# Optimization experiments

Measured on AMD Instinct MI355X. Metric: run time of the kernel, lower is better.

The kernel has to match this reference:

```python
import jax, jax.numpy as jnp
import numpy as np

N_NODES = 100000
N_EDGES = 1600000
N_GRAPHS = 64
D_IN, D_HID, D_LAT = 2, 64, 32


def setup_inputs() -> dict:
    key = jax.random.key(0)
    k1, k2, k3, k4, k5, k6, k7 = jax.random.split(key, 7)
    x = jax.random.normal(k1, (N_NODES, D_IN), dtype=jnp.float32)
    edge_index = jax.random.randint(k2, (2, N_EDGES), 0, N_NODES, dtype=jnp.int64)
    batch = jnp.sort(jax.random.randint(k3, (N_NODES,), 0, N_GRAPHS, dtype=jnp.int64))
    # GCNConv params (glorot-ish scale)
    W1 = jax.random.normal(k4, (D_IN, D_HID), dtype=jnp.float32) * (1.0 / np.sqrt(D_IN))
    b1 = jnp.zeros((D_HID,), dtype=jnp.float32)
    W2 = jax.random.normal(k5, (D_HID, D_LAT), dtype=jnp.float32) * (1.0 / np.sqrt(D_HID))
    b2 = jnp.zeros((D_LAT,), dtype=jnp.float32)
    return {"x": x, "W1": W1, "b1": b1, "W2": W2, "b2": b2,
            "edge_index": edge_index, "batch": batch}


def _gcn_conv(x, W, b, src, dst, n_nodes):
    """PyG GCNConv: add self-loops, symmetric deg^-1/2 normalization, linear, scatter-add."""
    h = x @ W  # [N, d_out]
    loop = jnp.arange(n_nodes, dtype=src.dtype)
    src_f = jnp.concatenate([src, loop])
    dst_f = jnp.concatenate([dst, loop])
    deg = jax.ops.segment_sum(jnp.ones_like(dst_f, dtype=h.dtype), dst_f,
                              num_segments=n_nodes)  # in-degree incl. self-loop
    dis = jnp.where(deg > 0, jax.lax.rsqrt(deg), 0.0)
    norm = dis[src_f] * dis[dst_f]  # [E+N]
    msg = h[src_f] * norm[:, None]  # edge gather (memory-bound)
    out = jax.ops.segment_sum(msg, dst_f, num_segments=n_nodes)
    return out + b


def reference(x, W1, b1, W2, b2, edge_index, batch):
    src, dst = edge_index[0], edge_index[1]
    n = x.shape[0]
    h = jax.nn.relu(_gcn_conv(x, W1, b1, src, dst, n))
    z = _gcn_conv(h, W2, b2, src, dst, n)
    # global_mean_pool over graph ids
    sums = jax.ops.segment_sum(z, batch, num_segments=N_GRAPHS)
    cnts = jax.ops.segment_sum(jnp.ones((n,), dtype=z.dtype), batch,
                               num_segments=N_GRAPHS)
    return sums / jnp.maximum(cnts, 1.0)[:, None]
```

## Files before the change

### kernel.cpp

```cpp
#include <hip/hip_runtime.h>
#include <hip/hip_fp16.h>

#define N_NODES  100000
#define N_EDGES  1600000
#define N_GRAPHS 64
#define NBUCK    391
#define NBLK     256
#define CHUNK    (N_EDGES / NBLK)
#define NODEBLK  1563

#define OFF_GSTART 0
#define OFF_ROWPTR 128
#define OFF_DIS    100224
#define OFF_S      200320
#define OFF_CSR    400384
#define OFF_QLO    2000384
#define OFF_QHI    2800512
#define OFF_BHIST  2000384
#define OFF_BOFFL  2100736
#define OFF_BSUM   2201088
#define OFF_BSTART 2201600
#define OFF_TMP    2202112

__device__ __forceinline__ int excl_scan_256(int v, int* wsum) {
  int t = threadIdx.x, lane = t & 63, w = t >> 6;
  int x = v;
#pragma unroll
  for (int off = 1; off < 64; off <<= 1) {
    int y = __shfl_up(x, off, 64);
    if (lane >= off) x += y;
  }
  if (lane == 63) wsum[w] = x;
  __syncthreads();
  if (t == 0) {
    int r = 0;
#pragma unroll
    for (int i = 0; i < 4; ++i) { int tv = wsum[i]; wsum[i] = r; r += tv; }
  }
  __syncthreads();
  return x - v + wsum[w];
}

__device__ __forceinline__ int excl_scan_512(int v, int* wsum) {
  int t = threadIdx.x, lane = t & 63, w = t >> 6;
  int x = v;
#pragma unroll
  for (int off = 1; off < 64; off <<= 1) {
    int y = __shfl_up(x, off, 64);
    if (lane >= off) x += y;
  }
  if (lane == 63) wsum[w] = x;
  __syncthreads();
  if (t == 0) {
    int r = 0;
#pragma unroll
    for (int i = 0; i < 8; ++i) { int tv = wsum[i]; wsum[i] = r; r += tv; }
  }
  __syncthreads();
  return x - v + wsum[w];
}

__global__ void k_hist(const int* __restrict__ dst, int* __restrict__ bhist) {
  __shared__ int hist[NBUCK];
  int t = threadIdx.x, k = blockIdx.x;
  for (int b = t; b < NBUCK; b += 256) hist[b] = 0;
  __syncthreads();
  int e0 = k * CHUNK, e1 = e0 + CHUNK;
  for (int e = e0 + t; e < e1; e += 256) atomicAdd(&hist[dst[e] >> 8], 1);
  __syncthreads();
  for (int b = t; b < NBUCK; b += 256) bhist[b * NBLK + k] = hist[b];
}

__global__ void k_scan_a(const int* __restrict__ bhist, int* __restrict__ boffl,
                         int* __restrict__ bsum, const int* __restrict__ batch,
                         int* __restrict__ gstart) {
  __shared__ int wsum[4];
  int t = threadIdx.x, b = blockIdx.x;
  int i = b * 256 + t;
  if (i < N_NODES) {
    int bi = batch[i];
    if (i == 0) {
      for (int g = 0; g <= bi; ++g) gstart[g] = 0;
    } else {
      int bp = batch[i - 1];
      for (int g = bp + 1; g <= bi; ++g) gstart[g] = i;
    }
    if (i == N_NODES - 1) {
      for (int g = bi + 1; g <= N_GRAPHS; ++g) gstart[g] = N_NODES;
    }
  }
  int v = bhist[b * NBLK + t];
  int ex = excl_scan_256(v, wsum);
  boffl[b * NBLK + t] = ex;
  if (t == NBLK - 1) bsum[b] = ex + v;
}

__global__ void k_scan_b(const int* __restrict__ bsum, int* __restrict__ bstart,
                         float* __restrict__ pooled) {
  __shared__ int wsum[8];
  int t = threadIdx.x;
  for (int i = t; i < N_GRAPHS * 32; i += 512) pooled[i] = 0.f;
  int v = (t < NBUCK) ? bsum[t] : 0;
  int ex = excl_scan_512(v, wsum);
  if (t <= NBUCK) bstart[t] = ex;
}

__global__ void k_scatter(const int* __restrict__ src, const int* __restrict__ dst,
                          const int* __restrict__ bstart, const int* __restrict__ boffl,
                          int* __restrict__ tmp) {
  __shared__ int sbase[NBUCK];
  __shared__ int fill[NBUCK];
  int t = threadIdx.x, k = blockIdx.x;
  for (int b = t; b < NBUCK; b += 256) {
    sbase[b] = bstart[b] + boffl[b * NBLK + k];
    fill[b] = 0;
  }
  __syncthreads();
  int e0 = k * CHUNK, e1 = e0 + CHUNK;
  for (int e = e0 + t; e < e1; e += 256) {
    int s_ = src[e], d_ = dst[e];
    int b = d_ >> 8;
    int pos = sbase[b] + atomicAdd(&fill[b], 1);
    tmp[pos] = (s_ << 8) | (d_ & 255);
  }
}

__global__ void k_fine(const int* __restrict__ tmp, const int* __restrict__ bstart,
                       const float* __restrict__ x, int* __restrict__ csr_src,
                       int* __restrict__ row_ptr, float* __restrict__ dis,
                       float2* __restrict__ s) {
  __shared__ int hist[256];
  __shared__ int fill[256];
  __shared__ int wsum[4];
  int t = threadIdx.x, b = blockIdx.x;
  int base_n = b << 8;
  int e0 = bstart[b], e1 = bstart[b + 1];
  hist[t] = 0;
  __syncthreads();
  for (int e = e0 + t; e < e1; e += 256) atomicAdd(&hist[tmp[e] & 255], 1);
  __syncthreads();
  int h = hist[t];
  int ex = excl_scan_256(h, wsum);
  hist[t] = ex;
  fill[t] = 0;
  int nn = min(256, N_NODES - base_n);
  if (t < nn) {
    int v = base_n + t;
    row_ptr[v] = e0 + ex;
    float dv = rsqrtf((float)(h + 1));
    dis[v] = dv;
    float2 xv = ((const float2*)x)[v];
    s[v] = make_float2(xv.x * dv, xv.y * dv);
  }
  if (b == NBUCK - 1 && t == 0) row_ptr[N_NODES] = e1;
  __syncthreads();
  for (int e = e0 + t; e < e1; e += 256) {
    int p = tmp[e];
    int fine = p & 255;
    int pos = e0 + hist[fine] + atomicAdd(&fill[fine], 1);
    csr_src[pos] = p >> 8;
  }
}

__global__ void k_layer1(const float2* __restrict__ s, const float* __restrict__ dis,
                         const int* __restrict__ row_ptr, const int* __restrict__ csr_src,
                         const float* __restrict__ W1, const float* __restrict__ b1,
                         const float* __restrict__ W2, int4* __restrict__ q_lo,
                         int4* __restrict__ q_hi) {
  __shared__ float4 sWB[64];
  __shared__ float4 sW2[512];
  int tid = threadIdx.x;
  if (tid < 64) sWB[tid] = make_float4(W1[tid], W1[64 + tid], b1[tid], 0.f);
  for (int i = tid; i < 512; i += 256) sW2[i] = ((const float4*)W2)[i];
  __syncthreads();
  int v = blockIdx.x * 256 + tid;
  if (v >= N_NODES) return;
  int beg = row_ptr[v], end = row_ptr[v + 1];
  float2 sv = s[v];
  float t0 = sv.x, t1 = sv.y;
  int k = beg;
  for (; k + 4 <= end; k += 4) {
    int u0 = csr_src[k], u1 = csr_src[k + 1], u2 = csr_src[k + 2], u3 = csr_src[k + 3];
    float2 a = s[u0], b = s[u1], c = s[u2], d = s[u3];
    t0 += (a.x + b.x) + (c.x + d.x);
    t1 += (a.y + b.y) + (c.y + d.y);
  }
  for (; k < end; ++k) {
    float2 su = s[csr_src[k]];
    t0 += su.x;
    t1 += su.y;
  }
  float dv = dis[v];
  t0 *= dv;
  t1 *= dv;
  float4 a4[8];
#pragma unroll
  for (int m = 0; m < 8; ++m) a4[m] = make_float4(0.f, 0.f, 0.f, 0.f);
  for (int j = 0; j < 64; ++j) {
    float4 wb = sWB[j];
    float r = fmaxf(fmaf(t0, wb.x, fmaf(t1, wb.y, wb.z)), 0.f);
#pragma unroll
    for (int m = 0; m < 8; ++m) {
      float4 w = sW2[j * 8 + m];
      a4[m].x = fmaf(r, w.x, a4[m].x);
      a4[m].y = fmaf(r, w.y, a4[m].y);
      a4[m].z = fmaf(r, w.z, a4[m].z);
      a4[m].w = fmaf(r, w.w, a4[m].w);
    }
  }
  int pk[16];
#pragma unroll
  for (int m = 0; m < 8; ++m) {
    __half2 h0 = __floats2half2_rn(a4[m].x * dv, a4[m].y * dv);
    __half2 h1 = __floats2half2_rn(a4[m].z * dv, a4[m].w * dv);
    pk[2 * m]     = *reinterpret_cast<int*>(&h0);
    pk[2 * m + 1] = *reinterpret_cast<int*>(&h1);
  }
  q_lo[v * 2]     = make_int4(pk[0], pk[1], pk[2], pk[3]);
  q_lo[v * 2 + 1] = make_int4(pk[4], pk[5], pk[6], pk[7]);
  q_hi[v * 2]     = make_int4(pk[8], pk[9], pk[10], pk[11]);
  q_hi[v * 2 + 1] = make_int4(pk[12], pk[13], pk[14], pk[15]);
}

__global__ void k_layer2(const __half2* __restrict__ q_lo, const __half2* __restrict__ q_hi,
                         const float* __restrict__ dis, const int* __restrict__ row_ptr,
                         const int* __restrict__ csr_src, const int* __restrict__ batch,
                         float* __restrict__ pooled) {
  __shared__ float2 red[32][8];
  int w = blockIdx.x;
  int h = (w & 7) >> 2;
  int sub = (w >> 3) * 4 + (w & 3);
  if (sub >= NODEBLK) return;
  const __half2* q = h ? q_hi : q_lo;
  int t = threadIdx.x;
  int fp = t & 7;
  int rg = t >> 3;
  int vb = sub * 64;
  int nlast = min(vb + 63, N_NODES - 1);
  bool uniform = (batch[vb] == batch[nlast]);
  int v0 = vb + rg * 2;
  int v1 = min(v0 + 2, N_NODES);
  float2 acc = make_float2(0.f, 0.f);
  int curg = (v0 < N_NODES) ? batch[v0] : -1;
  int obase = h * 16 + 2 * fp;
  for (int v = v0; v < v1; ++v) {
    if (!uniform) {
      int g = batch[v];
      if (g != curg) {
        atomicAdd(&pooled[curg * 32 + obase], acc.x);
        atomicAdd(&pooled[curg * 32 + obase + 1], acc.y);
        acc = make_float2(0.f, 0.f);
        curg = g;
      }
    }
    int e0 = row_ptr[v], e1 = row_ptr[v + 1];
    float2 z = __half22float2(q[v * 8 + fp]);
    int k = e0;
    for (; k + 8 <= e1; k += 8) {
      int u0 = csr_src[k],     u1 = csr_src[k + 1], u2 = csr_src[k + 2], u3 = csr_src[k + 3];
      int u4 = csr_src[k + 4], u5 = csr_src[k + 5], u6 = csr_src[k + 6], u7 = csr_src[k + 7];
      float2 f0 = __half22float2(q[u0 * 8 + fp]);
      float2 f1 = __half22float2(q[u1 * 8 + fp]);
      float2 f2 = __half22float2(q[u2 * 8 + fp]);
      float2 f3 = __half22float2(q[u3 * 8 + fp]);
      float2 f4 = __half22float2(q[u4 * 8 + fp]);
      float2 f5 = __half22float2(q[u5 * 8 + fp]);
      float2 f6 = __half22float2(q[u6 * 8 + fp]);
      float2 f7 = __half22float2(q[u7 * 8 + fp]);
      z.x += ((f0.x + f1.x) + (f2.x + f3.x)) + ((f4.x + f5.x) + (f6.x + f7.x));
      z.y += ((f0.y + f1.y) + (f2.y + f3.y)) + ((f4.y + f5.y) + (f6.y + f7.y));
    }
    for (; k + 4 <= e1; k += 4) {
      int u0 = csr_src[k], u1 = csr_src[k + 1], u2 = csr_src[k + 2], u3 = csr_src[k + 3];
      float2 f0 = __half22float2(q[u0 * 8 + fp]);
      float2 f1 = __half22float2(q[u1 * 8 + fp]);
      float2 f2 = __half22float2(q[u2 * 8 + fp]);
      float2 f3 = __half22float2(q[u3 * 8 + fp]);
      z.x += (f0.x + f1.x) + (f2.x + f3.x);
      z.y += (f0.y + f1.y) + (f2.y + f3.y);
    }
    for (; k < e1; ++k) {
      float2 f = __half22float2(q[csr_src[k] * 8 + fp]);
      z.x += f.x;
      z.y += f.y;
    }
    float dv = dis[v];
    acc.x = fmaf(z.x, dv, acc.x);
    acc.y = fmaf(z.y, dv, acc.y);
  }
  if (uniform) {
    red[rg][fp] = acc;
    __syncthreads();
    if (t < 8) {
      float2 ssum = make_float2(0.f, 0.f);
#pragma unroll
      for (int r = 0; r < 32; ++r) {
        ssum.x += red[r][t].x;
        ssum.y += red[r][t].y;
      }
      int g = batch[vb];
      atomicAdd(&pooled[g * 32 + h * 16 + 2 * t], ssum.x);
      atomicAdd(&pooled[g * 32 + h * 16 + 2 * t + 1], ssum.y);
    }
  } else if (curg >= 0) {
    atomicAdd(&pooled[curg * 32 + obase], acc.x);
    atomicAdd(&pooled[curg * 32 + obase + 1], acc.y);
  }
}

__global__ void k_final(float* __restrict__ out, const int* __restrict__ gstart,
                        const float* __restrict__ b2) {
  int i = blockIdx.x * 256 + threadIdx.x;
  if (i < N_GRAPHS * 32) {
    int g = i >> 5, l = i & 31;
    int c = gstart[g + 1] - gstart[g];
    out[i] = (c > 0) ? out[i] / (float)c + b2[l] : 0.f;
  }
}

extern "C" void kernel_launch(void* const* d_in, const int* in_sizes, int n_in,
                              void* d_out, int out_size, void* d_ws, size_t ws_size,
                              hipStream_t stream) {
  (void)in_sizes; (void)n_in; (void)out_size; (void)ws_size;
  const float* x   = (const float*)d_in[0];
  const float* W1  = (const float*)d_in[1];
  const float* b1  = (const float*)d_in[2];
  const float* W2  = (const float*)d_in[3];
  const float* b2  = (const float*)d_in[4];
  const int* edge  = (const int*)d_in[5];
  const int* batch = (const int*)d_in[6];
  const int* src = edge;
  const int* dst = edge + N_EDGES;
  float* out = (float*)d_out;

  int* ws      = (int*)d_ws;
  int* gstart  = ws + OFF_GSTART;
  int* row_ptr = ws + OFF_ROWPTR;
  float* dis   = (float*)(ws + OFF_DIS);
  float2* s    = (float2*)(ws + OFF_S);
  int* csr_src = ws + OFF_CSR;
  int4* q_lo4  = (int4*)(ws + OFF_QLO);
  int4* q_hi4  = (int4*)(ws + OFF_QHI);
  int* bhist   = ws + OFF_BHIST;
  int* boffl   = ws + OFF_BOFFL;
  int* bsum    = ws + OFF_BSUM;
  int* bstart  = ws + OFF_BSTART;
  int* tmp     = ws + OFF_TMP;

  k_hist<<<NBLK, 256, 0, stream>>>(dst, bhist);
  k_scan_a<<<NBUCK, 256, 0, stream>>>(bhist, boffl, bsum, batch, gstart);
  k_scan_b<<<1, 512, 0, stream>>>(bsum, bstart, out);
  k_scatter<<<NBLK, 256, 0, stream>>>(src, dst, bstart, boffl, tmp);
  k_fine<<<NBUCK, 256, 0, stream>>>(tmp, bstart, x, csr_src, row_ptr, dis, s);
  k_layer1<<<(N_NODES + 255) / 256, 256, 0, stream>>>(s, dis, row_ptr, csr_src,
                                                      W1, b1, W2, q_lo4, q_hi4);
  const int n_wg2 = ((NODEBLK + 3) / 4) * 8;
  k_layer2<<<n_wg2, 256, 0, stream>>>((const __half2*)q_lo4, (const __half2*)q_hi4,
                                      dis, row_ptr, csr_src, batch, out);
  k_final<<<8, 256, 0, stream>>>(out, gstart, b2);
}
```

Baseline: 105.4 us.

## Widen layer2 gathers to 8-byte half4 per thread, read weights directly in layer1

Layer 2 now assigns one node per 4-thread group, with each thread gathering 4 fp16 features (8 bytes) per neighbour instead of 2 features across 8 threads over two nodes. This halves the number of gather instructions and index loads per edge and drops the per-node batch-change loop. Layer 1 drops the shared-memory staging of W1/b1/W2 and reads the weights straight from global memory, expecting uniform scalar loads to hit cache. The trade-off is more registers per thread (32 accumulators) and possibly slower weight reads.

```diff
diff --git a/kernel.cpp b/kernel.cpp
--- a/kernel.cpp
+++ b/kernel.cpp
@@ -167,13 +167,7 @@
                          const float* __restrict__ W1, const float* __restrict__ b1,
                          const float* __restrict__ W2, int4* __restrict__ q_lo,
                          int4* __restrict__ q_hi) {
-  __shared__ float4 sWB[64];
-  __shared__ float4 sW2[512];
-  int tid = threadIdx.x;
-  if (tid < 64) sWB[tid] = make_float4(W1[tid], W1[64 + tid], b1[tid], 0.f);
-  for (int i = tid; i < 512; i += 256) sW2[i] = ((const float4*)W2)[i];
-  __syncthreads();
-  int v = blockIdx.x * 256 + tid;
+  int v = blockIdx.x * 256 + threadIdx.x;
   if (v >= N_NODES) return;
   int beg = row_ptr[v], end = row_ptr[v + 1];
   float2 sv = s[v];
@@ -193,28 +187,20 @@
   float dv = dis[v];
   t0 *= dv;
   t1 *= dv;
-  float4 a4[8];
-#pragma unroll
-  for (int m = 0; m < 8; ++m) a4[m] = make_float4(0.f, 0.f, 0.f, 0.f);
+  float acc[32];
+#pragma unroll
+  for (int m = 0; m < 32; ++m) acc[m] = 0.f;
+#pragma unroll 4
   for (int j = 0; j < 64; ++j) {
-    float4 wb = sWB[j];
-    float r = fmaxf(fmaf(t0, wb.x, fmaf(t1, wb.y, wb.z)), 0.f);
-#pragma unroll
-    for (int m = 0; m < 8; ++m) {
-      float4 w = sW2[j * 8 + m];
-      a4[m].x = fmaf(r, w.x, a4[m].x);
-      a4[m].y = fmaf(r, w.y, a4[m].y);
-      a4[m].z = fmaf(r, w.z, a4[m].z);
-      a4[m].w = fmaf(r, w.w, a4[m].w);
-    }
+    float r = fmaxf(fmaf(t0, W1[j], fmaf(t1, W1[64 + j], b1[j])), 0.f);
+#pragma unroll
+    for (int m = 0; m < 32; ++m) acc[m] = fmaf(r, W2[j * 32 + m], acc[m]);
   }
   int pk[16];
 #pragma unroll
-  for (int m = 0; m < 8; ++m) {
-    __half2 h0 = __floats2half2_rn(a4[m].x * dv, a4[m].y * dv);
-    __half2 h1 = __floats2half2_rn(a4[m].z * dv, a4[m].w * dv);
-    pk[2 * m]     = *reinterpret_cast<int*>(&h0);
-    pk[2 * m + 1] = *reinterpret_cast<int*>(&h1);
+  for (int m = 0; m < 16; ++m) {
+    __half2 h = __floats2half2_rn(acc[2 * m] * dv, acc[2 * m + 1] * dv);
+    pk[m] = *reinterpret_cast<int*>(&h);
   }
   q_lo[v * 2]     = make_int4(pk[0], pk[1], pk[2], pk[3]);
   q_lo[v * 2 + 1] = make_int4(pk[4], pk[5], pk[6], pk[7]);
@@ -222,89 +208,92 @@
   q_hi[v * 2 + 1] = make_int4(pk[12], pk[13], pk[14], pk[15]);
 }
 
-__global__ void k_layer2(const __half2* __restrict__ q_lo, const __half2* __restrict__ q_hi,
+__device__ __forceinline__ float4 qunpack(uint2 p) {
+  __half2 h0 = *reinterpret_cast<__half2*>(&p.x);
+  __half2 h1 = *reinterpret_cast<__half2*>(&p.y);
+  float2 a = __half22float2(h0), b = __half22float2(h1);
+  return make_float4(a.x, a.y, b.x, b.y);
+}
+
+__global__ void k_layer2(const uint2* __restrict__ q_lo, const uint2* __restrict__ q_hi,
                          const float* __restrict__ dis, const int* __restrict__ row_ptr,
                          const int* __restrict__ csr_src, const int* __restrict__ batch,
                          float* __restrict__ pooled) {
-  __shared__ float2 red[32][8];
+  __shared__ float4 red[64][4];
   int w = blockIdx.x;
   int h = (w & 7) >> 2;
   int sub = (w >> 3) * 4 + (w & 3);
   if (sub >= NODEBLK) return;
-  const __half2* q = h ? q_hi : q_lo;
+  const uint2* q = h ? q_hi : q_lo;
   int t = threadIdx.x;
-  int fp = t & 7;
-  int rg = t >> 3;
+  int fp = t & 3;
+  int rg = t >> 2;
   int vb = sub * 64;
+  int v = vb + rg;
   int nlast = min(vb + 63, N_NODES - 1);
   bool uniform = (batch[vb] == batch[nlast]);
-  int v0 = vb + rg * 2;
-  int v1 = min(v0 + 2, N_NODES);
-  float2 acc = make_float2(0.f, 0.f);
-  int curg = (v0 < N_NODES) ? batch[v0] : -1;
-  int obase = h * 16 + 2 * fp;
-  for (int v = v0; v < v1; ++v) {
-    if (!uniform) {
-      int g = batch[v];
-      if (g != curg) {
-        atomicAdd(&pooled[curg * 32 + obase], acc.x);
-        atomicAdd(&pooled[curg * 32 + obase + 1], acc.y);
-        acc = make_float2(0.f, 0.f);
-        curg = g;
-      }
-    }
+  float4 acc = make_float4(0.f, 0.f, 0.f, 0.f);
+  int g = -1;
+  if (v < N_NODES) {
+    g = batch[v];
     int e0 = row_ptr[v], e1 = row_ptr[v + 1];
-    float2 z = __half22float2(q[v * 8 + fp]);
+    float4 z = qunpack(q[v * 4 + fp]);
     int k = e0;
     for (; k + 8 <= e1; k += 8) {
       int u0 = csr_src[k],     u1 = csr_src[k + 1], u2 = csr_src[k + 2], u3 = csr_src[k + 3];
       int u4 = csr_src[k + 4], u5 = csr_src[k + 5], u6 = csr_src[k + 6], u7 = csr_src[k + 7];
-      float2 f0 = __half22float2(q[u0 * 8 + fp]);
-      float2 f1 = __half22float2(q[u1 * 8 + fp]);
-      float2 f2 = __half22float2(q[u2 * 8 + fp]);
-      float2 f3 = __half22float2(q[u3 * 8 + fp]);
-      float2 f4 = __half22float2(q[u4 * 8 + fp]);
-      float2 f5 = __half22float2(q[u5 * 8 + fp]);
-      float2 f6 = __half22float2(q[u6 * 8 + fp]);
-      float2 f7 = __half22float2(q[u7 * 8 + fp]);
+      float4 f0 = qunpack(q[u0 * 4 + fp]);
+      float4 f1 = qunpack(q[u1 * 4 + fp]);
+      float4 f2 = qunpack(q[u2 * 4 + fp]);
+      float4 f3 = qunpack(q[u3 * 4 + fp]);
+      float4 f4 = qunpack(q[u4 * 4 + fp]);
+      float4 f5 = qunpack(q[u5 * 4 + fp]);
+      float4 f6 = qunpack(q[u6 * 4 + fp]);
+      float4 f7 = qunpack(q[u7 * 4 + fp]);
       z.x += ((f0.x + f1.x) + (f2.x + f3.x)) + ((f4.x + f5.x) + (f6.x + f7.x));
       z.y += ((f0.y + f1.y) + (f2.y + f3.y)) + ((f4.y + f5.y) + (f6.y + f7.y));
-    }
-    for (; k + 4 <= e1; k += 4) {
-      int u0 = csr_src[k], u1 = csr_src[k + 1], u2 = csr_src[k + 2], u3 = csr_src[k + 3];
-      float2 f0 = __half22float2(q[u0 * 8 + fp]);
-      float2 f1 = __half22float2(q[u1 * 8 + fp]);
-      float2 f2 = __half22float2(q[u2 * 8 + fp]);
-      float2 f3 = __half22float2(q[u3 * 8 + fp]);
-      z.x += (f0.x + f1.x) + (f2.x + f3.x);
-      z.y += (f0.y + f1.y) + (f2.y + f3.y);
+      z.z += ((f0.z + f1.z) + (f2.z + f3.z)) + ((f4.z + f5.z) + (f6.z + f7.z));
+      z.w += ((f0.w + f1.w) + (f2.w + f3.w)) + ((f4.w + f5.w) + (f6.w + f7.w));
+    }
+    for (; k + 2 <= e1; k += 2) {
+      int u0 = csr_src[k], u1 = csr_src[k + 1];
+      float4 f0 = qunpack(q[u0 * 4 + fp]);
+      float4 f1 = qunpack(q[u1 * 4 + fp]);
+      z.x += f0.x + f1.x;
+      z.y += f0.y + f1.y;
+      z.z += f0.z + f1.z;
+      z.w += f0.w + f1.w;
     }
     for (; k < e1; ++k) {
-      float2 f = __half22float2(q[csr_src[k] * 8 + fp]);
-      z.x += f.x;
-      z.y += f.y;
-    }
-    float dv = dis[v];
-    acc.x = fmaf(z.x, dv, acc.x);
-    acc.y = fmaf(z.y, dv, acc.y);
+      float4 f = qunpack(q[csr_src[k] * 4 + fp]);
+      z.x += f.x; z.y += f.y; z.z += f.z; z.w += f.w;
+    }
+    float dvv = dis[v];
+    acc = make_float4(z.x * dvv, z.y * dvv, z.z * dvv, z.w * dvv);
   }
   if (uniform) {
     red[rg][fp] = acc;
     __syncthreads();
-    if (t < 8) {
-      float2 ssum = make_float2(0.f, 0.f);
-#pragma unroll
-      for (int r = 0; r < 32; ++r) {
-        ssum.x += red[r][t].x;
-        ssum.y += red[r][t].y;
+    if (t < 4) {
+      float4 ssum = make_float4(0.f, 0.f, 0.f, 0.f);
+#pragma unroll
+      for (int r = 0; r < 64; ++r) {
+        float4 x4 = red[r][t];
+        ssum.x += x4.x; ssum.y += x4.y; ssum.z += x4.z; ssum.w += x4.w;
       }
-      int g = batch[vb];
-      atomicAdd(&pooled[g * 32 + h * 16 + 2 * t], ssum.x);
-      atomicAdd(&pooled[g * 32 + h * 16 + 2 * t + 1], ssum.y);
-    }
-  } else if (curg >= 0) {
-    atomicAdd(&pooled[curg * 32 + obase], acc.x);
-    atomicAdd(&pooled[curg * 32 + obase + 1], acc.y);
+      int gg = batch[vb];
+      int base = gg * 32 + h * 16 + t * 4;
+      atomicAdd(&pooled[base],     ssum.x);
+      atomicAdd(&pooled[base + 1], ssum.y);
+      atomicAdd(&pooled[base + 2], ssum.z);
+      atomicAdd(&pooled[base + 3], ssum.w);
+    }
+  } else if (v < N_NODES) {
+    int base = g * 32 + h * 16 + fp * 4;
+    atomicAdd(&pooled[base],     acc.x);
+    atomicAdd(&pooled[base + 1], acc.y);
+    atomicAdd(&pooled[base + 2], acc.z);
+    atomicAdd(&pooled[base + 3], acc.w);
   }
 }
 
@@ -355,7 +344,7 @@
   k_layer1<<<(N_NODES + 255) / 256, 256, 0, stream>>>(s, dis, row_ptr, csr_src,
                                                       W1, b1, W2, q_lo4, q_hi4);
   const int n_wg2 = ((NODEBLK + 3) / 4) * 8;
-  k_layer2<<<n_wg2, 256, 0, stream>>>((const __half2*)q_lo4, (const __half2*)q_hi4,
+  k_layer2<<<n_wg2, 256, 0, stream>>>((const uint2*)q_lo4, (const uint2*)q_hi4,
                                       dis, row_ptr, csr_src, batch, out);
   k_final<<<8, 256, 0, stream>>>(out, gstart, b2);
 }
```

Result: slower. 114.9 us (+9.1%).

## Store layer-2 features as FP8 and gather all 32 channels in one pass

Applied to the files above, without the earlier changes.

Layer-1 output features are packed into FP8 (32 bytes per node) instead of two FP16 halves, and layer 2 now decodes 4 channels per thread in one pass over the edges instead of two separate half-feature passes. This halves the random-gather bytes per edge and removes the duplicate traversal of CSR indices. The cost is a large loss of precision in the message features, which may exceed tolerance. The 4-wide unrolled remainder loop is also dropped.

```diff
diff --git a/kernel.cpp b/kernel.cpp
--- a/kernel.cpp
+++ b/kernel.cpp
@@ -14,13 +14,14 @@
 #define OFF_DIS    100224
 #define OFF_S      200320
 #define OFF_CSR    400384
-#define OFF_QLO    2000384
-#define OFF_QHI    2800512
+#define OFF_Q      2000384
 #define OFF_BHIST  2000384
 #define OFF_BOFFL  2100736
 #define OFF_BSUM   2201088
 #define OFF_BSTART 2201600
 #define OFF_TMP    2202112
+
+typedef float fvec2 __attribute__((ext_vector_type(2)));
 
 __device__ __forceinline__ int excl_scan_256(int v, int* wsum) {
   int t = threadIdx.x, lane = t & 63, w = t >> 6;
@@ -165,8 +166,7 @@
 __global__ void k_layer1(const float2* __restrict__ s, const float* __restrict__ dis,
                          const int* __restrict__ row_ptr, const int* __restrict__ csr_src,
                          const float* __restrict__ W1, const float* __restrict__ b1,
-                         const float* __restrict__ W2, int4* __restrict__ q_lo,
-                         int4* __restrict__ q_hi) {
+                         const float* __restrict__ W2, int4* __restrict__ q8) {
   __shared__ float4 sWB[64];
   __shared__ float4 sW2[512];
   int tid = threadIdx.x;
@@ -208,103 +208,102 @@
       a4[m].w = fmaf(r, w.w, a4[m].w);
     }
   }
-  int pk[16];
+  int pk[8];
 #pragma unroll
   for (int m = 0; m < 8; ++m) {
-    __half2 h0 = __floats2half2_rn(a4[m].x * dv, a4[m].y * dv);
-    __half2 h1 = __floats2half2_rn(a4[m].z * dv, a4[m].w * dv);
-    pk[2 * m]     = *reinterpret_cast<int*>(&h0);
-    pk[2 * m + 1] = *reinterpret_cast<int*>(&h1);
-  }
-  q_lo[v * 2]     = make_int4(pk[0], pk[1], pk[2], pk[3]);
-  q_lo[v * 2 + 1] = make_int4(pk[4], pk[5], pk[6], pk[7]);
-  q_hi[v * 2]     = make_int4(pk[8], pk[9], pk[10], pk[11]);
-  q_hi[v * 2 + 1] = make_int4(pk[12], pk[13], pk[14], pk[15]);
-}
-
-__global__ void k_layer2(const __half2* __restrict__ q_lo, const __half2* __restrict__ q_hi,
-                         const float* __restrict__ dis, const int* __restrict__ row_ptr,
-                         const int* __restrict__ csr_src, const int* __restrict__ batch,
-                         float* __restrict__ pooled) {
-  __shared__ float2 red[32][8];
-  int w = blockIdx.x;
-  int h = (w & 7) >> 2;
-  int sub = (w >> 3) * 4 + (w & 3);
-  if (sub >= NODEBLK) return;
-  const __half2* q = h ? q_hi : q_lo;
+    int wrd = __builtin_amdgcn_cvt_pk_fp8_f32(a4[m].x * dv, a4[m].y * dv, 0, false);
+    wrd = __builtin_amdgcn_cvt_pk_fp8_f32(a4[m].z * dv, a4[m].w * dv, wrd, true);
+    pk[m] = wrd;
+  }
+  q8[v * 2]     = make_int4(pk[0], pk[1], pk[2], pk[3]);
+  q8[v * 2 + 1] = make_int4(pk[4], pk[5], pk[6], pk[7]);
+}
+
+__device__ __forceinline__ float4 qdec(unsigned int d) {
+  fvec2 lo = __builtin_amdgcn_cvt_pk_f32_fp8(d, false);
+  fvec2 hi = __builtin_amdgcn_cvt_pk_f32_fp8(d, true);
+  return make_float4(lo.x, lo.y, hi.x, hi.y);
+}
+
+__global__ void k_layer2(const unsigned int* __restrict__ q, const float* __restrict__ dis,
+                         const int* __restrict__ row_ptr, const int* __restrict__ csr_src,
+                         const int* __restrict__ batch, float* __restrict__ pooled) {
+  __shared__ float4 red[32][9];
   int t = threadIdx.x;
   int fp = t & 7;
   int rg = t >> 3;
-  int vb = sub * 64;
+  int vb = blockIdx.x * 64;
   int nlast = min(vb + 63, N_NODES - 1);
   bool uniform = (batch[vb] == batch[nlast]);
   int v0 = vb + rg * 2;
   int v1 = min(v0 + 2, N_NODES);
-  float2 acc = make_float2(0.f, 0.f);
+  float4 acc = make_float4(0.f, 0.f, 0.f, 0.f);
   int curg = (v0 < N_NODES) ? batch[v0] : -1;
-  int obase = h * 16 + 2 * fp;
   for (int v = v0; v < v1; ++v) {
     if (!uniform) {
       int g = batch[v];
       if (g != curg) {
-        atomicAdd(&pooled[curg * 32 + obase], acc.x);
-        atomicAdd(&pooled[curg * 32 + obase + 1], acc.y);
-        acc = make_float2(0.f, 0.f);
+        int base = curg * 32 + fp * 4;
+        atomicAdd(&pooled[base],     acc.x);
+        atomicAdd(&pooled[base + 1], acc.y);
+        atomicAdd(&pooled[base + 2], acc.z);
+        atomicAdd(&pooled[base + 3], acc.w);
+        acc = make_float4(0.f, 0.f, 0.f, 0.f);
         curg = g;
       }
     }
     int e0 = row_ptr[v], e1 = row_ptr[v + 1];
-    float2 z = __half22float2(q[v * 8 + fp]);
+    float4 z = qdec(q[v * 8 + fp]);
     int k = e0;
     for (; k + 8 <= e1; k += 8) {
       int u0 = csr_src[k],     u1 = csr_src[k + 1], u2 = csr_src[k + 2], u3 = csr_src[k + 3];
       int u4 = csr_src[k + 4], u5 = csr_src[k + 5], u6 = csr_src[k + 6], u7 = csr_src[k + 7];
-      float2 f0 = __half22float2(q[u0 * 8 + fp]);
-      float2 f1 = __half22float2(q[u1 * 8 + fp]);
-      float2 f2 = __half22float2(q[u2 * 8 + fp]);
-      float2 f3 = __half22float2(q[u3 * 8 + fp]);
-      float2 f4 = __half22float2(q[u4 * 8 + fp]);
-      float2 f5 = __half22float2(q[u5 * 8 + fp]);
-      float2 f6 = __half22float2(q[u6 * 8 + fp]);
-      float2 f7 = __half22float2(q[u7 * 8 + fp]);
+      float4 f0 = qdec(q[u0 * 8 + fp]);
+      float4 f1 = qdec(q[u1 * 8 + fp]);
+      float4 f2 = qdec(q[u2 * 8 + fp]);
+      float4 f3 = qdec(q[u3 * 8 + fp]);
+      float4 f4 = qdec(q[u4 * 8 + fp]);
+      float4 f5 = qdec(q[u5 * 8 + fp]);
+      float4 f6 = qdec(q[u6 * 8 + fp]);
+      float4 f7 = qdec(q[u7 * 8 + fp]);
       z.x += ((f0.x + f1.x) + (f2.x + f3.x)) + ((f4.x + f5.x) + (f6.x + f7.x));
       z.y += ((f0.y + f1.y) + (f2.y + f3.y)) + ((f4.y + f5.y) + (f6.y + f7.y));
-    }
-    for (; k + 4 <= e1; k += 4) {
-      int u0 = csr_src[k], u1 = csr_src[k + 1], u2 = csr_src[k + 2], u3 = csr_src[k + 3];
-      float2 f0 = __half22float2(q[u0 * 8 + fp]);
-      float2 f1 = __half22float2(q[u1 * 8 + fp]);
-      float2 f2 = __half22float2(q[u2 * 8 + fp]);
-      float2 f3 = __half22float2(q[u3 * 8 + fp]);
-      z.x += (f0.x + f1.x) + (f2.x + f3.x);
-      z.y += (f0.y + f1.y) + (f2.y + f3.y);
+      z.z += ((f0.z + f1.z) + (f2.z + f3.z)) + ((f4.z + f5.z) + (f6.z + f7.z));
+      z.w += ((f0.w + f1.w) + (f2.w + f3.w)) + ((f4.w + f5.w) + (f6.w + f7.w));
     }
     for (; k < e1; ++k) {
-      float2 f = __half22float2(q[csr_src[k] * 8 + fp]);
-      z.x += f.x;
-      z.y += f.y;
-    }
-    float dv = dis[v];
-    acc.x = fmaf(z.x, dv, acc.x);
-    acc.y = fmaf(z.y, dv, acc.y);
+      float4 f = qdec(q[csr_src[k] * 8 + fp]);
+      z.x += f.x; z.y += f.y; z.z += f.z; z.w += f.w;
+    }
+    float dvv = dis[v];
+    acc.x = fmaf(z.x, dvv, acc.x);
+    acc.y = fmaf(z.y, dvv, acc.y);
+    acc.z = fmaf(z.z, dvv, acc.z);
+    acc.w = fmaf(z.w, dvv, acc.w);
   }
   if (uniform) {
     red[rg][fp] = acc;
     __syncthreads();
     if (t < 8) {
-      float2 ssum = make_float2(0.f, 0.f);
+      float4 ssum = make_float4(0.f, 0.f, 0.f, 0.f);
 #pragma unroll
       for (int r = 0; r < 32; ++r) {
-        ssum.x += red[r][t].x;
-        ssum.y += red[r][t].y;
+        float4 x4 = red[r][t];
+        ssum.x += x4.x; ssum.y += x4.y; ssum.z += x4.z; ssum.w += x4.w;
       }
-      int g = batch[vb];
-      atomicAdd(&pooled[g * 32 + h * 16 + 2 * t], ssum.x);
-      atomicAdd(&pooled[g * 32 + h * 16 + 2 * t + 1], ssum.y);
-    }
-  } else if (curg >= 0) {
-    atomicAdd(&pooled[curg * 32 + obase], acc.x);
-    atomicAdd(&pooled[curg * 32 + obase + 1], acc.y);
+      int gg = batch[vb];
+      int base = gg * 32 + t * 4;
+      atomicAdd(&pooled[base],     ssum.x);
+      atomicAdd(&pooled[base + 1], ssum.y);
+      atomicAdd(&pooled[base + 2], ssum.z);
+      atomicAdd(&pooled[base + 3], ssum.w);
+    }
+  } else if (v0 < N_NODES) {
+    int base = curg * 32 + fp * 4;
+    atomicAdd(&pooled[base],     acc.x);
+    atomicAdd(&pooled[base + 1], acc.y);
+    atomicAdd(&pooled[base + 2], acc.z);
+    atomicAdd(&pooled[base + 3], acc.w);
   }
 }
 
@@ -339,8 +338,7 @@
   float* dis   = (float*)(ws + OFF_DIS);
   float2* s    = (float2*)(ws + OFF_S);
   int* csr_src = ws + OFF_CSR;
-  int4* q_lo4  = (int4*)(ws + OFF_QLO);
-  int4* q_hi4  = (int4*)(ws + OFF_QHI);
+  int4* q8     = (int4*)(ws + OFF_Q);
   int* bhist   = ws + OFF_BHIST;
   int* boffl   = ws + OFF_BOFFL;
   int* bsum    = ws + OFF_BSUM;
@@ -353,9 +351,8 @@
   k_scatter<<<NBLK, 256, 0, stream>>>(src, dst, bstart, boffl, tmp);
   k_fine<<<NBUCK, 256, 0, stream>>>(tmp, bstart, x, csr_src, row_ptr, dis, s);
   k_layer1<<<(N_NODES + 255) / 256, 256, 0, stream>>>(s, dis, row_ptr, csr_src,
-                                                      W1, b1, W2, q_lo4, q_hi4);
-  const int n_wg2 = ((NODEBLK + 3) / 4) * 8;
-  k_layer2<<<n_wg2, 256, 0, stream>>>((const __half2*)q_lo4, (const __half2*)q_hi4,
-                                      dis, row_ptr, csr_src, batch, out);
+                                                      W1, b1, W2, q8);
+  k_layer2<<<NODEBLK, 256, 0, stream>>>((const unsigned int*)q8, dis, row_ptr,
+                                        csr_src, batch, out);
   k_final<<<8, 256, 0, stream>>>(out, gstart, b2);
 }
```

Measured after the change: 97.16 us. -7.8%, faster.
